# Kernel optimization log

Hardware: AMD Instinct MI355X
Metric: run time of the kernel (lower is better)

Reference implementation:

```python
import jax, jax.numpy as jnp
import numpy as np

# w_mul = gain * 5**-0.5 * lrmul with gain=sqrt(2), use_wscale=True, lrmul=1
W_MUL = float(2 ** 0.5 * 5 ** -0.5)


def _apply_1q(M, g, q):
    """Apply 2x2 gate g on qubit q (MSB-first) to the rows of matrix M (dim, dim)."""
    dim = M.shape[0]
    Mr = M.reshape(2 ** q, 2, -1)  # (pre, 2, post*dim)
    return jnp.einsum('ab,xby->xay', g, Mr).reshape(dim, dim)


def _fused_xyz_gates(th, n):
    """Per-qubit fused gate Rz(tz) @ Ry(ty) @ Rx(tx); th = [tx_0..n, ty_0..n, tz_0..n]."""
    hx, hy, hz = th[:n] / 2, th[n:2 * n] / 2, th[2 * n:] / 2
    cx, sx = jnp.cos(hx), jnp.sin(hx)
    cy, sy = jnp.cos(hy), jnp.sin(hy)
    z = jnp.zeros_like(hz)
    gx = jnp.stack([jnp.stack([cx + 0j, -1j * sx], -1),
                    jnp.stack([-1j * sx, cx + 0j], -1)], -2)
    gy = jnp.stack([jnp.stack([cy + 0j, -sy + 0j], -1),
                    jnp.stack([sy + 0j, cy + 0j], -1)], -2)
    ez = jnp.exp(-1j * hz)
    gz = jnp.stack([jnp.stack([ez, z + 0j], -1),
                    jnp.stack([z + 0j, jnp.conj(ez)], -1)], -2)
    return jnp.einsum('nab,nbc,ncd->nad', gz, gy, gx).astype(jnp.complex64)


def _cnot_perm(n, c, t):
    """Row permutation implementing CNOT(control=c, target=t), MSB-first bit order."""
    r = np.arange(2 ** n)
    return r ^ (((r >> (n - 1 - c)) & 1) << (n - 1 - t))


def _build_U(weight):
    n = weight.shape[0] // 15
    dim = 2 ** n
    w = weight * W_MUL
    ring_perms = [jnp.asarray(_cnot_perm(n, c, (c + 1) % n)) for c in range(n)]
    U = jnp.eye(dim, dtype=jnp.complex64)
    for layer in range(5):  # 5 XYZ layers, rings of CNOT between them
        g = _fused_xyz_gates(w[3 * n * layer:3 * n * (layer + 1)], n)
        for q in range(n):
            U = _apply_1q(U, g[q], q)
        if layer < 4:
            for p in ring_perms:
                U = U[p]  # CNOT is a row permutation
    return U


def setup_inputs() -> dict:
    key = jax.random.key(0)
    k1, k2 = jax.random.split(key)
    n_qubits = 11
    dim = 2 ** n_qubits
    x = jax.random.normal(k1, (dim, dim), dtype=jnp.float32)
    weight = jax.random.uniform(k2, (15 * n_qubits,), dtype=jnp.float32,
                                minval=0.0, maxval=2.0 * np.pi)
    return {"x": x, "weight": weight}


def reference(x, weight):
    U = _build_U(weight)
    xc = x.astype(jnp.complex64)
    return U @ xc @ U.conj().T
```

## Files before the change

### kernel.cpp

```cpp
#include <hip/hip_runtime.h>

typedef unsigned short u16;
typedef __attribute__((ext_vector_type(8))) short bf16x8;
typedef __attribute__((ext_vector_type(4))) float f32x4;
typedef __attribute__((ext_vector_type(4))) unsigned int u32x4;

#define DIM 2048

__device__ inline u16 f2bf(float f) {
    unsigned u = __builtin_bit_cast(unsigned, f);
    u = (u + 0x7FFFu + ((u >> 16) & 1u)) >> 16;
    return (u16)u;
}

__device__ inline void gl_lds16(const void* g, void* l) {
    __builtin_amdgcn_global_load_lds(
        (const __attribute__((address_space(1))) unsigned int*)g,
        (__attribute__((address_space(3))) unsigned int*)l, 16, 0, 0);
}

struct c32 { float x, y; };
__device__ inline c32 cmul(c32 a, c32 b) { return {a.x*b.x - a.y*b.y, a.x*b.y + a.y*b.x}; }
__device__ inline float2 cmulf2(float2 a, float2 b) {
    return make_float2(a.x*b.x - a.y*b.y, a.x*b.y + a.y*b.x);
}

__device__ inline int slot2(int i) { return i + (i >> 4); }

template<int M>
__device__ inline float2 swzx2(float2 v) {
    int x = __builtin_amdgcn_ds_swizzle(__builtin_bit_cast(int, v.x), (M << 10) | 0x1F);
    int y = __builtin_amdgcn_ds_swizzle(__builtin_bit_cast(int, v.y), (M << 10) | 0x1F);
    return make_float2(__builtin_bit_cast(float, x), __builtin_bit_cast(float, y));
}

__device__ inline void bfly(float2 g0, float2 g1, float2 g2, float2 g3,
                            float2& u, float2& w) {
    float2 nu, nw;
    nu.x = g0.x*u.x - g0.y*u.y + g1.x*w.x - g1.y*w.y;
    nu.y = g0.x*u.y + g0.y*u.x + g1.x*w.y + g1.y*w.x;
    nw.x = g2.x*u.x - g2.y*u.y + g3.x*w.x - g3.y*w.y;
    nw.y = g2.x*u.y + g2.y*u.x + g3.x*w.y + g3.y*w.x;
    u = nu; w = nw;
}

__global__ __launch_bounds__(256, 4) void build_ut(const float* __restrict__ w,
                                                   u16* __restrict__ ut_re,
                                                   u16* __restrict__ ut_im) {
    __shared__ alignas(16) float2 gg[55][4];
    __shared__ alignas(16) float2 V[2][DIM + (DIM >> 4)];
    const int tid  = threadIdx.x;
    const int lane = tid & 63;
    const int col0 = blockIdx.x * 2;

    if (tid < 55) {
        const int layer = tid / 11, q = tid - layer * 11;
        const float WM = 0.63245553203367586f;
        float hx = 0.5f * WM * w[33*layer + q];
        float hy = 0.5f * WM * w[33*layer + 11 + q];
        float hz = 0.5f * WM * w[33*layer + 22 + q];
        float cx = cosf(hx), sx = sinf(hx);
        float cy = cosf(hy), sy = sinf(hy);
        float cz = cosf(hz), sz = sinf(hz);
        c32 m00{cy*cx,  sy*sx}, m01{-sy*cx, -cy*sx};
        c32 m10{sy*cx, -cy*sx}, m11{ cy*cx, -sy*sx};
        c32 em{cz, -sz}, ep{cz, sz};
        c32 r0 = cmul(em, m00), r1 = cmul(em, m01);
        c32 r2 = cmul(ep, m10), r3 = cmul(ep, m11);
        gg[tid][0] = make_float2(r0.x, r0.y);
        gg[tid][1] = make_float2(r1.x, r1.y);
        gg[tid][2] = make_float2(r2.x, r2.y);
        gg[tid][3] = make_float2(r3.x, r3.y);
    }
    __syncthreads();

    #pragma unroll
    for (int c = 0; c < 2; ++c) {
        const int col = col0 + c;
        float2 p = gg[0][((((tid >> 7) & 1) << 1)) | ((col >> 10) & 1)];
        #pragma unroll
        for (int b = 9; b >= 3; --b) {
            float2 ge = gg[10 - b][(((tid >> (b - 3)) & 1) << 1) | ((col >> b) & 1)];
            p = cmulf2(p, ge);
        }
        const int c2 = (col >> 2) & 1, c1 = (col >> 1) & 1, c0 = col & 1;
        float2 a0  = cmulf2(p, gg[8][c2]);
        float2 a1  = cmulf2(p, gg[8][2 | c2]);
        float2 b00 = cmulf2(a0, gg[9][c1]);
        float2 b01 = cmulf2(a0, gg[9][2 | c1]);
        float2 b10 = cmulf2(a1, gg[9][c1]);
        float2 b11 = cmulf2(a1, gg[9][2 | c1]);
        float2 g0 = gg[10][c0], g1 = gg[10][2 | c0];
        const int sb = slot2(tid << 3);
        V[c][sb + 0] = cmulf2(b00, g0);
        V[c][sb + 1] = cmulf2(b00, g1);
        V[c][sb + 2] = cmulf2(b01, g0);
        V[c][sb + 3] = cmulf2(b01, g1);
        V[c][sb + 4] = cmulf2(b10, g0);
        V[c][sb + 5] = cmulf2(b10, g1);
        V[c][sb + 6] = cmulf2(b11, g0);
        V[c][sb + 7] = cmulf2(b11, g1);
    }
    __syncthreads();

    for (int layer = 1; layer < 5; ++layer) {
        const int gb = layer * 11;

        auto tri = [&](float2 (&a)[8], int gq) {
            {   float2 g0 = gg[gq][0], g1 = gg[gq][1], g2 = gg[gq][2], g3 = gg[gq][3];
                bfly(g0,g1,g2,g3, a[0], a[4]); bfly(g0,g1,g2,g3, a[1], a[5]);
                bfly(g0,g1,g2,g3, a[2], a[6]); bfly(g0,g1,g2,g3, a[3], a[7]); }
            {   float2 g0 = gg[gq+1][0], g1 = gg[gq+1][1], g2 = gg[gq+1][2], g3 = gg[gq+1][3];
                bfly(g0,g1,g2,g3, a[0], a[2]); bfly(g0,g1,g2,g3, a[1], a[3]);
                bfly(g0,g1,g2,g3, a[4], a[6]); bfly(g0,g1,g2,g3, a[5], a[7]); }
            {   float2 g0 = gg[gq+2][0], g1 = gg[gq+2][1], g2 = gg[gq+2][2], g3 = gg[gq+2][3];
                bfly(g0,g1,g2,g3, a[0], a[1]); bfly(g0,g1,g2,g3, a[2], a[3]);
                bfly(g0,g1,g2,g3, a[4], a[5]); bfly(g0,g1,g2,g3, a[6], a[7]); }
        };

        {
            float2 a0[8], a1[8]; int sl[8];
            #pragma unroll
            for (int j = 0; j < 8; ++j) {
                int e  = tid | (j << 8);
                sl[j]  = slot2(e);
                int pe = (e ^ (e >> 1)) ^ ((e & 1) ? 0x600 : 0);
                int ps = slot2(pe);
                a0[j] = V[0][ps];
                a1[j] = V[1][ps];
            }
            __syncthreads();
            tri(a0, gb + 0);
            tri(a1, gb + 0);
            #pragma unroll
            for (int j = 0; j < 8; ++j) { V[0][sl[j]] = a0[j]; V[1][sl[j]] = a1[j]; }
            __syncthreads();
        }

        {
            const int sb = slot2(tid << 3);
            float2 v0[8], v1[8];
            #pragma unroll
            for (int j = 0; j < 8; ++j) { v0[j] = V[0][sb + j]; v1[j] = V[1][sb + j]; }

            auto lane_gate = [&](int gq, int M, auto swz) {
                const bool hi = (lane & M) != 0;
                float2 g0 = gg[gq][0], g1 = gg[gq][1], g2 = gg[gq][2], g3 = gg[gq][3];
                float2 ca = hi ? g3 : g0;
                float2 cb = hi ? g2 : g1;
                #pragma unroll
                for (int j = 0; j < 8; ++j) {
                    float2 p = swz(v0[j]);
                    float2 o = v0[j];
                    v0[j].x = ca.x*o.x - ca.y*o.y + cb.x*p.x - cb.y*p.y;
                    v0[j].y = ca.x*o.y + ca.y*o.x + cb.x*p.y + cb.y*p.x;
                    float2 q = swz(v1[j]);
                    float2 u = v1[j];
                    v1[j].x = ca.x*u.x - ca.y*u.y + cb.x*q.x - cb.y*q.y;
                    v1[j].y = ca.x*u.y + ca.y*u.x + cb.x*q.y + cb.y*q.x;
                }
            };
            lane_gate(gb + 3, 16, [](float2 t){ return swzx2<16>(t); });
            lane_gate(gb + 4,  8, [](float2 t){ return swzx2< 8>(t); });
            lane_gate(gb + 5,  4, [](float2 t){ return swzx2< 4>(t); });
            lane_gate(gb + 6,  2, [](float2 t){ return swzx2< 2>(t); });
            lane_gate(gb + 7,  1, [](float2 t){ return swzx2< 1>(t); });

            tri(v0, gb + 8);
            tri(v1, gb + 8);

            if (layer < 4) {
                #pragma unroll
                for (int j = 0; j < 8; ++j) { V[0][sb + j] = v0[j]; V[1][sb + j] = v1[j]; }
                __syncthreads();
            } else {
                const int base = tid << 3;
                u32x4 pr, pi;
                pr.x = (unsigned)f2bf(v0[0].x) | ((unsigned)f2bf(v0[1].x) << 16);
                pr.y = (unsigned)f2bf(v0[2].x) | ((unsigned)f2bf(v0[3].x) << 16);
                pr.z = (unsigned)f2bf(v0[4].x) | ((unsigned)f2bf(v0[5].x) << 16);
                pr.w = (unsigned)f2bf(v0[6].x) | ((unsigned)f2bf(v0[7].x) << 16);
                pi.x = (unsigned)f2bf(v0[0].y) | ((unsigned)f2bf(v0[1].y) << 16);
                pi.y = (unsigned)f2bf(v0[2].y) | ((unsigned)f2bf(v0[3].y) << 16);
                pi.z = (unsigned)f2bf(v0[4].y) | ((unsigned)f2bf(v0[5].y) << 16);
                pi.w = (unsigned)f2bf(v0[6].y) | ((unsigned)f2bf(v0[7].y) << 16);
                *(u32x4*)(ut_re + (size_t)col0 * DIM + base) = pr;
                *(u32x4*)(ut_im + (size_t)col0 * DIM + base) = pi;
                pr.x = (unsigned)f2bf(v1[0].x) | ((unsigned)f2bf(v1[1].x) << 16);
                pr.y = (unsigned)f2bf(v1[2].x) | ((unsigned)f2bf(v1[3].x) << 16);
                pr.z = (unsigned)f2bf(v1[4].x) | ((unsigned)f2bf(v1[5].x) << 16);
                pr.w = (unsigned)f2bf(v1[6].x) | ((unsigned)f2bf(v1[7].x) << 16);
                pi.x = (unsigned)f2bf(v1[0].y) | ((unsigned)f2bf(v1[1].y) << 16);
                pi.y = (unsigned)f2bf(v1[2].y) | ((unsigned)f2bf(v1[3].y) << 16);
                pi.z = (unsigned)f2bf(v1[4].y) | ((unsigned)f2bf(v1[5].y) << 16);
                pi.w = (unsigned)f2bf(v1[6].y) | ((unsigned)f2bf(v1[7].y) << 16);
                *(u32x4*)(ut_re + (size_t)(col0 + 1) * DIM + base) = pr;
                *(u32x4*)(ut_im + (size_t)(col0 + 1) * DIM + base) = pi;
            }
        }
    }
}

__global__ __launch_bounds__(256) void transpose2(const u16* __restrict__ sre,
                                                  const u16* __restrict__ sim,
                                                  u16* __restrict__ dre,
                                                  u16* __restrict__ dim_,
                                                  const float* __restrict__ x,
                                                  u16* __restrict__ xb) {
    const int bx = blockIdx.x * 64, by = blockIdx.y * 64;
    if (blockIdx.z == 2) {
        for (int e = threadIdx.x; e < 512; e += 256) {
            int r = e >> 3, c8 = (e & 7) * 8;
            const float4* s4 = (const float4*)(x + (size_t)(by + r) * DIM + bx + c8);
            float4 v0 = s4[0], v1 = s4[1];
            u32x4 pk;
            pk.x = (unsigned)f2bf(v0.x) | ((unsigned)f2bf(v0.y) << 16);
            pk.y = (unsigned)f2bf(v0.z) | ((unsigned)f2bf(v0.w) << 16);
            pk.z = (unsigned)f2bf(v1.x) | ((unsigned)f2bf(v1.y) << 16);
            pk.w = (unsigned)f2bf(v1.z) | ((unsigned)f2bf(v1.w) << 16);
            *(u32x4*)(xb + (size_t)(by + r) * DIM + bx + c8) = pk;
        }
        return;
    }
    const u16* s = blockIdx.z ? sim : sre;
    u16*       d = blockIdx.z ? dim_ : dre;
    __shared__ alignas(16) u16 tile[64][66];
    for (int e = threadIdx.x; e < 1024; e += 256) {
        int r = e >> 4, c4 = (e & 15) * 4;
        uint2 v = *(const uint2*)(s + (size_t)(by + r) * DIM + bx + c4);
        u16* tp = &tile[r][c4];
        tp[0] = (u16)(v.x); tp[1] = (u16)(v.x >> 16);
        tp[2] = (u16)(v.y); tp[3] = (u16)(v.y >> 16);
    }
    __syncthreads();
    for (int e = threadIdx.x; e < 1024; e += 256) {
        int r = e >> 4, c4 = (e & 15) * 4;
        unsigned lo = (unsigned)tile[c4][r]     | ((unsigned)tile[c4+1][r] << 16);
        unsigned hi = (unsigned)tile[c4+2][r]   | ((unsigned)tile[c4+3][r] << 16);
        *(uint2*)(d + (size_t)(bx + r) * DIM + by + c4) = make_uint2(lo, hi);
    }
}

__global__ __launch_bounds__(256, 2) void gemm_stage1(
        const u16* __restrict__ uStack,
        const u16* __restrict__ xb,
        u16* __restrict__ ptStack) {
    __shared__ alignas(16) u16 Ab[2][2][128*32], Bx[2][2][128*32];
    const int tid  = threadIdx.x;
    const int lane = tid & 63, w = tid >> 6;
    const int m0 = blockIdx.y * 128, n0 = blockIdx.x * 128;
    const int wm = (w >> 1) * 64, wn = (w & 1) * 64;
    const int ml = lane & 15, quad = lane >> 4;

    f32x4 acc[4][4];
    #pragma unroll
    for (int i = 0; i < 4; ++i)
        #pragma unroll
        for (int j = 0; j < 4; ++j) {
            f32x4 z = {0.f, 0.f, 0.f, 0.f};
            acc[i][j] = z;
        }

    auto stage = [&](int b, int k0) {
        #pragma unroll
        for (int pn = 0; pn < 2; ++pn) {
            #pragma unroll
            for (int t = 0; t < 2; ++t) {
                int ci = t * 256 + tid;
                int r = ci >> 2, c = ci & 3;
                size_t goA = ((size_t)(m0 + r) * DIM + k0 + pn * 32) * 2 + c * 16;
                size_t goB = ((size_t)(n0 + r) * DIM + k0 + pn * 32) * 2 + c * 16;
                gl_lds16((const char*)uStack + goA, (char*)Ab[b][pn] + ci * 16);
                gl_lds16((const char*)xb     + goB, (char*)Bx[b][pn] + ci * 16);
            }
        }
    };

    stage(0, 0);
    __syncthreads();

    for (int k0 = 0; k0 < DIM; k0 += 64) {
        const int cb = (k0 >> 6) & 1;
        if (k0 + 64 < DIM) stage(cb ^ 1, k0 + 64);

        #pragma unroll
        for (int pn = 0; pn < 2; ++pn) {
            bf16x8 af[4], bf[4];
            #pragma unroll
            for (int i = 0; i < 4; ++i) {
                af[i] = *(const bf16x8*)(Ab[cb][pn] + (wm + i*16 + ml) * 32 + quad * 8);
                bf[i] = *(const bf16x8*)(Bx[cb][pn] + (wn + i*16 + ml) * 32 + quad * 8);
            }
            #pragma unroll
            for (int i = 0; i < 4; ++i)
                #pragma unroll
                for (int j = 0; j < 4; ++j)
                    acc[i][j] = __builtin_amdgcn_mfma_f32_16x16x32_bf16(af[i], bf[j], acc[i][j], 0, 0, 0);
        }
        __syncthreads();
    }
    #pragma unroll
    for (int i = 0; i < 4; ++i)
        #pragma unroll
        for (int j = 0; j < 4; ++j) {
            int row = m0 + wm + i*16 + quad*4;
            int col = n0 + wn + j*16 + ml;
            #pragma unroll
            for (int r = 0; r < 4; ++r)
                ptStack[(size_t)(row + r) * DIM + col] = f2bf(acc[i][j][r]);
        }
}

__global__ __launch_bounds__(256, 2) void gemm_stage2_fused(
        const u16* __restrict__ ure, const u16* __restrict__ uim,
        const u16* __restrict__ pt, const u16* __restrict__ qt,
        float* __restrict__ out) {
    __shared__ alignas(16) u16 Ab[2][2][128*32], Bb[2][2][64*32];
    const int tid  = threadIdx.x;
    const int lane = tid & 63, w = tid >> 6;
    const int m0 = blockIdx.y * 128, n0 = blockIdx.x * 64;
    const int wm = (w >> 1) * 64, wn = (w & 1) * 32;
    const int ml = lane & 15, quad = lane >> 4;

    f32x4 acc[4][2];
    #pragma unroll
    for (int i = 0; i < 4; ++i)
        #pragma unroll
        for (int j = 0; j < 2; ++j) {
            f32x4 z = {0.f, 0.f, 0.f, 0.f};
            acc[i][j] = z;
        }

    auto stage = [&](int b, int kk) {
        const u16* A = (kk & DIM) ? uim : ure;
        const u16* B = (kk & DIM) ? qt  : pt;
        const int k0 = kk & (DIM - 1);
        #pragma unroll
        for (int pn = 0; pn < 2; ++pn) {
            #pragma unroll
            for (int t = 0; t < 2; ++t) {
                int ci = t * 256 + tid;
                int r = ci >> 2, c = ci & 3;
                size_t goA = ((size_t)(m0 + r) * DIM + k0 + pn * 32) * 2 + c * 16;
                gl_lds16((const char*)A + goA, (char*)Ab[b][pn] + ci * 16);
            }
            {
                int r = tid >> 2, c = tid & 3;
                size_t goB = ((size_t)(n0 + r) * DIM + k0 + pn * 32) * 2 + c * 16;
                gl_lds16((const char*)B + goB, (char*)Bb[b][pn] + tid * 16);
            }
        }
    };

    stage(0, 0);
    __syncthreads();

    for (int kk = 0; kk < 2 * DIM; kk += 64) {
        const int cb = (kk >> 6) & 1;
        if (kk + 64 < 2 * DIM) stage(cb ^ 1, kk + 64);

        #pragma unroll
        for (int pn = 0; pn < 2; ++pn) {
            bf16x8 af[4], bf[2];
            #pragma unroll
            for (int i = 0; i < 4; ++i)
                af[i] = *(const bf16x8*)(Ab[cb][pn] + (wm + i*16 + ml) * 32 + quad * 8);
            #pragma unroll
            for (int j = 0; j < 2; ++j)
                bf[j] = *(const bf16x8*)(Bb[cb][pn] + (wn + j*16 + ml) * 32 + quad * 8);
            #pragma unroll
            for (int i = 0; i < 4; ++i)
                #pragma unroll
                for (int j = 0; j < 2; ++j)
                    acc[i][j] = __builtin_amdgcn_mfma_f32_16x16x32_bf16(af[i], bf[j], acc[i][j], 0, 0, 0);
        }
        __syncthreads();
    }
    #pragma unroll
    for (int i = 0; i < 4; ++i)
        #pragma unroll
        for (int j = 0; j < 2; ++j) {
            int row = m0 + wm + i*16 + quad*4;
            int col = n0 + wn + j*16 + ml;
            #pragma unroll
            for (int r = 0; r < 4; ++r)
                out[(size_t)(row + r) * DIM + col] = acc[i][j][r];
        }
}

__global__ __launch_bounds__(256, 1) void gemm_stage2_cplx(
        const u16* __restrict__ ure, const u16* __restrict__ uim,
        const u16* __restrict__ pt, const u16* __restrict__ qt,
        float2* __restrict__ out, size_t out_lim) {
    __shared__ alignas(16) u16 Ar[128*32], Ai[128*32], Bp[128*32], Bq[128*32];
    const int tid  = threadIdx.x;
    const int lane = tid & 63, w = tid >> 6;
    const int m0 = blockIdx.y * 128, n0 = blockIdx.x * 128;
    const int wm = (w >> 1) * 64, wn = (w & 1) * 64;
    const int ml = lane & 15, quad = lane >> 4;

    f32x4 accR[4][4], accI[4][4];
    #pragma unroll
    for (int i = 0; i < 4; ++i)
        #pragma unroll
        for (int j = 0; j < 4; ++j) {
            f32x4 z = {0.f, 0.f, 0.f, 0.f};
            accR[i][j] = z; accI[i][j] = z;
        }

    for (int k0 = 0; k0 < DIM; k0 += 32) {
        #pragma unroll
        for (int t = 0; t < 2; ++t) {
            int ci = t * 256 + tid;
            int r = ci >> 2, c = ci & 3;
            size_t goA = ((size_t)(m0 + r) * DIM + k0) * 2 + c * 16;
            size_t goB = ((size_t)(n0 + r) * DIM + k0) * 2 + c * 16;
            gl_lds16((const char*)ure + goA, (char*)Ar + ci * 16);
            gl_lds16((const char*)uim + goA, (char*)Ai + ci * 16);
            gl_lds16((const char*)pt  + goB, (char*)Bp + ci * 16);
            gl_lds16((const char*)qt  + goB, (char*)Bq + ci * 16);
        }
        __syncthreads();
        bf16x8 ar[4], ai[4], bp[4], bq[4];
        #pragma unroll
        for (int i = 0; i < 4; ++i) {
            ar[i] = *(const bf16x8*)(Ar + (wm + i*16 + ml) * 32 + quad * 8);
            ai[i] = *(const bf16x8*)(Ai + (wm + i*16 + ml) * 32 + quad * 8);
            bp[i] = *(const bf16x8*)(Bp + (wn + i*16 + ml) * 32 + quad * 8);
            bq[i] = *(const bf16x8*)(Bq + (wn + i*16 + ml) * 32 + quad * 8);
        }
        #pragma unroll
        for (int i = 0; i < 4; ++i)
            #pragma unroll
            for (int j = 0; j < 4; ++j) {
                accR[i][j] = __builtin_amdgcn_mfma_f32_16x16x32_bf16(ar[i], bp[j], accR[i][j], 0, 0, 0);
                accR[i][j] = __builtin_amdgcn_mfma_f32_16x16x32_bf16(ai[i], bq[j], accR[i][j], 0, 0, 0);
                accI[i][j] = __builtin_amdgcn_mfma_f32_16x16x32_bf16(ai[i], bp[j], accI[i][j], 0, 0, 0);
                f32x4 t2 = __builtin_amdgcn_mfma_f32_16x16x32_bf16(ar[i], bq[j], {0.f,0.f,0.f,0.f}, 0, 0, 0);
                accI[i][j] -= t2;
            }
        __syncthreads();
    }
    #pragma unroll
    for (int i = 0; i < 4; ++i)
        #pragma unroll
        for (int j = 0; j < 4; ++j) {
            int row = m0 + wm + i*16 + quad*4;
            int col = n0 + wn + j*16 + ml;
            #pragma unroll
            for (int r = 0; r < 4; ++r) {
                size_t idx = (size_t)(row + r) * DIM + col;
                if (idx < out_lim)
                    out[idx] = make_float2(accR[i][j][r], accI[i][j][r]);
            }
        }
}

extern "C" void kernel_launch(void* const* d_in, const int* in_sizes, int n_in,
                              void* d_out, int out_size, void* d_ws, size_t ws_size,
                              hipStream_t stream) {
    int xi = (in_sizes[0] >= in_sizes[1]) ? 0 : 1;
    const float* x = (const float*)d_in[xi];
    const float* w = (const float*)d_in[1 - xi];

    char* ws = (char*)d_ws;
    const size_t P = (size_t)DIM * DIM * 2;
    if (ws_size < 4 * P) return;

    u16* ut_re = (u16*)(ws);
    u16* ut_im = (u16*)(ws + P);
    u16* u_re  = (u16*)(ws + 2*P);
    u16* u_im  = (u16*)(ws + 3*P);
    u16* pt    = ut_re;
    u16* qt    = ut_im;
    u16* xb = (ws_size >= 5 * P) ? (u16*)(ws + 4*P) : (u16*)d_out;

    build_ut<<<DIM/2, 256, 0, stream>>>(w, ut_re, ut_im);
    transpose2<<<dim3(32, 32, 3), 256, 0, stream>>>(ut_re, ut_im, u_re, u_im, x, xb);
    gemm_stage1<<<dim3(16, 32), 256, 0, stream>>>(u_re, xb, pt);

    if (out_size == DIM * DIM) {
        gemm_stage2_fused<<<dim3(32, 16), 256, 0, stream>>>(u_re, u_im, pt, qt,
                                                            (float*)d_out);
    } else {
        gemm_stage2_cplx<<<dim3(16, 16), 256, 0, stream>>>(u_re, u_im, pt, qt,
                                                           (float2*)d_out,
                                                           (size_t)out_size / 2);
    }
}
```

Before: 239.0 us.

## Compute first CNOT-permuted layer directly in registers and remap GEMM block order for XCD locality

The U-building kernel no longer writes the layer-0 product state to LDS and reads it back through the CNOT-ring permutation. Instead, layer 1 computes the permuted amplitudes straight into registers from factored per-qubit gate products, which removes one LDS round trip and a barrier. Both GEMM kernels also remap the linear block index so that consecutive blocks (likely spread round-robin across the chiplets) get contiguous tiles, aiming for better L2 reuse. The closed-form permutation indexing is intricate and easy to get wrong, and the U-build stage is a small part of total time.

```diff
diff --git a/kernel.cpp b/kernel.cpp
--- a/kernel.cpp
+++ b/kernel.cpp
@@ -74,35 +74,6 @@
     }
     __syncthreads();
 
-    #pragma unroll
-    for (int c = 0; c < 2; ++c) {
-        const int col = col0 + c;
-        float2 p = gg[0][((((tid >> 7) & 1) << 1)) | ((col >> 10) & 1)];
-        #pragma unroll
-        for (int b = 9; b >= 3; --b) {
-            float2 ge = gg[10 - b][(((tid >> (b - 3)) & 1) << 1) | ((col >> b) & 1)];
-            p = cmulf2(p, ge);
-        }
-        const int c2 = (col >> 2) & 1, c1 = (col >> 1) & 1, c0 = col & 1;
-        float2 a0  = cmulf2(p, gg[8][c2]);
-        float2 a1  = cmulf2(p, gg[8][2 | c2]);
-        float2 b00 = cmulf2(a0, gg[9][c1]);
-        float2 b01 = cmulf2(a0, gg[9][2 | c1]);
-        float2 b10 = cmulf2(a1, gg[9][c1]);
-        float2 b11 = cmulf2(a1, gg[9][2 | c1]);
-        float2 g0 = gg[10][c0], g1 = gg[10][2 | c0];
-        const int sb = slot2(tid << 3);
-        V[c][sb + 0] = cmulf2(b00, g0);
-        V[c][sb + 1] = cmulf2(b00, g1);
-        V[c][sb + 2] = cmulf2(b01, g0);
-        V[c][sb + 3] = cmulf2(b01, g1);
-        V[c][sb + 4] = cmulf2(b10, g0);
-        V[c][sb + 5] = cmulf2(b10, g1);
-        V[c][sb + 6] = cmulf2(b11, g0);
-        V[c][sb + 7] = cmulf2(b11, g1);
-    }
-    __syncthreads();
-
     for (int layer = 1; layer < 5; ++layer) {
         const int gb = layer * 11;
 
@@ -121,15 +92,52 @@
         {
             float2 a0[8], a1[8]; int sl[8];
             #pragma unroll
-            for (int j = 0; j < 8; ++j) {
-                int e  = tid | (j << 8);
-                sl[j]  = slot2(e);
-                int pe = (e ^ (e >> 1)) ^ ((e & 1) ? 0x600 : 0);
-                int ps = slot2(pe);
-                a0[j] = V[0][ps];
-                a1[j] = V[1][ps];
-            }
-            __syncthreads();
+            for (int j = 0; j < 8; ++j) sl[j] = slot2(tid | (j << 8));
+
+            if (layer == 1) {
+                const int t0 = tid & 1, t7 = (tid >> 7) & 1;
+                const int L  = (tid ^ (tid >> 1)) & 0x7F;
+                float2 Ps = gg[9][(((L >> 1) & 1) << 1) | ((col0 >> 1) & 1)];
+                #pragma unroll
+                for (int b = 2; b <= 6; ++b)
+                    Ps = cmulf2(Ps, gg[10 - b][(((L >> b) & 1) << 1) | ((col0 >> b) & 1)]);
+                float2 P0 = cmulf2(Ps, gg[10][(L & 1) << 1]);
+                float2 P1 = cmulf2(Ps, gg[10][((L & 1) << 1) | 1]);
+                const int c7 = (col0 >> 7) & 1, c8 = (col0 >> 8) & 1;
+                const int c9 = (col0 >> 9) & 1, c10 = (col0 >> 10) & 1;
+                float2 B4[2][2], A40[2][2], A41[2][2];
+                #pragma unroll
+                for (int j0 = 0; j0 < 2; ++j0)
+                    #pragma unroll
+                    for (int j1 = 0; j1 < 2; ++j1)
+                        B4[j0][j1] = cmulf2(gg[3][((t7 ^ j0) << 1) | c7],
+                                            gg[2][((j0 ^ j1) << 1) | c8]);
+                #pragma unroll
+                for (int j1 = 0; j1 < 2; ++j1)
+                    #pragma unroll
+                    for (int j2 = 0; j2 < 2; ++j2) {
+                        float2 A4 = cmulf2(gg[1][((j1 ^ j2 ^ t0) << 1) | c9],
+                                           gg[0][((j2 ^ t0) << 1) | c10]);
+                        A40[j1][j2] = cmulf2(A4, P0);
+                        A41[j1][j2] = cmulf2(A4, P1);
+                    }
+                #pragma unroll
+                for (int j = 0; j < 8; ++j) {
+                    const int j0 = j & 1, j1 = (j >> 1) & 1, j2 = (j >> 2) & 1;
+                    a0[j] = cmulf2(B4[j0][j1], A40[j1][j2]);
+                    a1[j] = cmulf2(B4[j0][j1], A41[j1][j2]);
+                }
+            } else {
+                #pragma unroll
+                for (int j = 0; j < 8; ++j) {
+                    int e  = tid | (j << 8);
+                    int pe = (e ^ (e >> 1)) ^ ((e & 1) ? 0x600 : 0);
+                    int ps = slot2(pe);
+                    a0[j] = V[0][ps];
+                    a1[j] = V[1][ps];
+                }
+                __syncthreads();
+            }
             tri(a0, gb + 0);
             tri(a1, gb + 0);
             #pragma unroll
@@ -248,7 +256,9 @@
     __shared__ alignas(16) u16 Ab[2][2][128*32], Bx[2][2][128*32];
     const int tid  = threadIdx.x;
     const int lane = tid & 63, w = tid >> 6;
-    const int m0 = blockIdx.y * 128, n0 = blockIdx.x * 128;
+    const int lin = blockIdx.y * 16 + blockIdx.x;
+    const int t   = (lin & 7) * 64 + (lin >> 3);
+    const int m0 = (t >> 4) * 128, n0 = (t & 15) * 128;
     const int wm = (w >> 1) * 64, wn = (w & 1) * 64;
     const int ml = lane & 15, quad = lane >> 4;
 
@@ -265,8 +275,8 @@
         #pragma unroll
         for (int pn = 0; pn < 2; ++pn) {
             #pragma unroll
-            for (int t = 0; t < 2; ++t) {
-                int ci = t * 256 + tid;
+            for (int t2 = 0; t2 < 2; ++t2) {
+                int ci = t2 * 256 + tid;
                 int r = ci >> 2, c = ci & 3;
                 size_t goA = ((size_t)(m0 + r) * DIM + k0 + pn * 32) * 2 + c * 16;
                 size_t goB = ((size_t)(n0 + r) * DIM + k0 + pn * 32) * 2 + c * 16;
@@ -318,7 +328,9 @@
     __shared__ alignas(16) u16 Ab[2][2][128*32], Bb[2][2][64*32];
     const int tid  = threadIdx.x;
     const int lane = tid & 63, w = tid >> 6;
-    const int m0 = blockIdx.y * 128, n0 = blockIdx.x * 64;
+    const int lin = blockIdx.y * 32 + blockIdx.x;
+    const int t   = (lin & 7) * 64 + (lin >> 3);
+    const int m0 = (t >> 5) * 128, n0 = (t & 31) * 64;
     const int wm = (w >> 1) * 64, wn = (w & 1) * 32;
     const int ml = lane & 15, quad = lane >> 4;
 
@@ -338,8 +350,8 @@
         #pragma unroll
         for (int pn = 0; pn < 2; ++pn) {
             #pragma unroll
-            for (int t = 0; t < 2; ++t) {
-                int ci = t * 256 + tid;
+            for (int t2 = 0; t2 < 2; ++t2) {
+                int ci = t2 * 256 + tid;
                 int r = ci >> 2, c = ci & 3;
                 size_t goA = ((size_t)(m0 + r) * DIM + k0 + pn * 32) * 2 + c * 16;
                 gl_lds16((const char*)A + goA, (char*)Ab[b][pn] + ci * 16);
```

After: 243.1 us. Within noise of the previous version (+1.7%).
